# Kernel tuning notes

Measured on AMD Instinct MI355X. Metric: run time of the kernel, lower is better.

Reference implementation:

```python
import jax, jax.numpy as jnp
import numpy as np

B, S, D, H = 4, 2048, 1024, 16
HD = D // H  # head_dim = 64


def setup_inputs() -> dict:
    key = jax.random.key(0)
    ks = jax.random.split(key, 10)
    scale = 1.0 / np.sqrt(D)
    x = jax.random.normal(ks[0], (B, S, D), dtype=jnp.float32)
    mask = jax.random.randint(ks[1], (B, S, S), 0, 2, dtype=jnp.int32)
    Wq = jax.random.normal(ks[2], (D, D), dtype=jnp.float32) * scale
    Wk = jax.random.normal(ks[3], (D, D), dtype=jnp.float32) * scale
    Wv = jax.random.normal(ks[4], (D, D), dtype=jnp.float32) * scale
    Wo = jax.random.normal(ks[5], (D, D), dtype=jnp.float32) * scale
    bq = jax.random.normal(ks[6], (D,), dtype=jnp.float32) * 0.01
    bk = jax.random.normal(ks[7], (D,), dtype=jnp.float32) * 0.01
    bv = jax.random.normal(ks[8], (D,), dtype=jnp.float32) * 0.01
    bo = jax.random.normal(ks[9], (D,), dtype=jnp.float32) * 0.01
    return {"x": x, "mask": mask, "Wq": Wq, "bq": bq, "Wk": Wk, "bk": bk,
            "Wv": Wv, "bv": bv, "Wo": Wo, "bo": bo}


def reference(x, mask, Wq, bq, Wk, bk, Wv, bv, Wo, bo):
    # QKV projections (nn.Linear: x @ W^T + b; W stored pre-transposed here as [D,D])
    q = x @ Wq + bq  # [B,S,D]
    k = x @ Wk + bk
    v = x @ Wv + bv
    # split heads -> [B,H,S,HD]
    def heads(t):
        return t.reshape(B, S, H, HD).transpose(0, 2, 1, 3)
    q, k, v = heads(q), heads(k), heads(v)
    scores = jnp.einsum('bhqd,bhkd->bhqk', q, k) / jnp.sqrt(jnp.float32(HD))
    # mask: [B,S,S] -> broadcast over heads; positions where mask==0 get -inf
    scores = jnp.where(mask[:, None, :, :] == 0, -jnp.inf, scores)
    attn = jax.nn.softmax(scores, axis=-1)
    attn = jnp.where(jnp.isnan(attn), 0.0, attn)  # nan_to_num(nan=0.0)
    out = jnp.einsum('bhqk,bhkd->bhqd', attn, v)  # [B,H,S,HD]
    out = out.transpose(0, 2, 1, 3).reshape(B, S, D)
    return out @ Wo + bo
```

## Files before the change

### kernel.cpp

```cpp
#include <hip/hip_runtime.h>
#include <hip/hip_bf16.h>
#include <stdint.h>

#define B_  4
#define S_  2048
#define D_  1024
#define H_  16
#define HD_ 64

typedef __attribute__((ext_vector_type(4))) float f32x4;
typedef __attribute__((ext_vector_type(8))) short bf16x8;

typedef const unsigned int __attribute__((address_space(1)))* gas_ptr;
typedef unsigned int __attribute__((address_space(3)))* las_ptr;

__device__ __forceinline__ void async16(const void* g, void* l) {
  __builtin_amdgcn_global_load_lds((gas_ptr)g, (las_ptr)l, 16, 0, 0);
}

__global__ __launch_bounds__(256) void cvt_x(const float* __restrict__ in,
                                             __hip_bfloat16* __restrict__ out,
                                             int n) {
  const int i = (blockIdx.x * blockDim.x + threadIdx.x) * 4;
  if (i >= n) return;
  const float4 v = *(const float4*)(in + i);
  union { ushort4 u; __hip_bfloat16 h[4]; } o;
  o.h[0] = (__hip_bfloat16)v.x;
  o.h[1] = (__hip_bfloat16)v.y;
  o.h[2] = (__hip_bfloat16)v.z;
  o.h[3] = (__hip_bfloat16)v.w;
  *(ushort4*)(out + i) = o.u;
}

__global__ __launch_bounds__(256) void pack_mask(const int* __restrict__ mk,
                                                 unsigned long long* __restrict__ bits) {
  const long long i = (long long)blockIdx.x * 256 + threadIdx.x;
  const unsigned long long b = __ballot(mk[i] != 0);
  if ((threadIdx.x & 63) == 0) bits[i >> 6] = b;
}

__global__ void transpose_w(const float* __restrict__ Wq,
                            const float* __restrict__ Wk,
                            const float* __restrict__ Wv,
                            const float* __restrict__ Wo,
                            __hip_bfloat16* __restrict__ Wt_qkv,
                            __hip_bfloat16* __restrict__ Wt_o) {
  __shared__ float t[32][33];
  const int z = blockIdx.z;
  const float* W = (z == 0) ? Wq : (z == 1) ? Wk : (z == 2) ? Wv : Wo;
  __hip_bfloat16* Wt = (z < 3) ? (Wt_qkv + (size_t)z * D_ * D_) : Wt_o;
  const int x = blockIdx.x * 32 + threadIdx.x;
  const int y = blockIdx.y * 32 + threadIdx.y;
  t[threadIdx.y][threadIdx.x] = W[(size_t)y * D_ + x];
  __syncthreads();
  const int xo = blockIdx.y * 32 + threadIdx.x;
  const int yo = blockIdx.x * 32 + threadIdx.y;
  Wt[(size_t)yo * D_ + xo] = (__hip_bfloat16)t[threadIdx.x][threadIdx.y];
}

__global__ __launch_bounds__(256) void gemm_qkv(
    const __hip_bfloat16* __restrict__ A,
    const __hip_bfloat16* __restrict__ Bt,
    const float* __restrict__ bq,
    const float* __restrict__ bk,
    const float* __restrict__ bv,
    __hip_bfloat16* __restrict__ QKo,
    __hip_bfloat16* __restrict__ Vt) {
  __shared__ __hip_bfloat16 sA[128 * 32];
  __shared__ __hip_bfloat16 sB[128 * 32];
  const int K = 1024;
  const int tid  = threadIdx.x;
  const int wave = tid >> 6;
  const int lane = tid & 63;
  const int quad = lane >> 4;
  const int l16  = lane & 15;
  const int bm = blockIdx.y * 128;
  const int bn = blockIdx.x * 128;
  const int wm = (wave >> 1) * 64;
  const int wn = (wave & 1) * 64;

  const int r0 = wave * 2, r1 = wave * 2 + 1;
  const int lrow = lane >> 2;
  const int lcol = (lane & 3) * 8;

  const __hip_bfloat16* ga0 = A  + (size_t)(bm + r0 * 16 + lrow) * K + lcol;
  const __hip_bfloat16* ga1 = A  + (size_t)(bm + r1 * 16 + lrow) * K + lcol;
  const __hip_bfloat16* gb0 = Bt + (size_t)(bn + r0 * 16 + lrow) * K + lcol;
  const __hip_bfloat16* gb1 = Bt + (size_t)(bn + r1 * 16 + lrow) * K + lcol;
  char* la0 = (char*)sA + r0 * 1024;
  char* la1 = (char*)sA + r1 * 1024;
  char* lb0 = (char*)sB + r0 * 1024;
  char* lb1 = (char*)sB + r1 * 1024;

  const char* pa = (const char*)sA + (wm + l16) * 64 + quad * 16;
  const char* pb = (const char*)sB + (wn + l16) * 64 + quad * 16;

  f32x4 acc[4][4] = {};

  for (int k0 = 0; k0 < K; k0 += 32) {
    async16(ga0 + k0, la0);
    async16(ga1 + k0, la1);
    async16(gb0 + k0, lb0);
    async16(gb1 + k0, lb1);
    __syncthreads();
    bf16x8 af[4], bf[4];
#pragma unroll
    for (int mt = 0; mt < 4; ++mt) af[mt] = *(const bf16x8*)(pa + mt * 1024);
#pragma unroll
    for (int nt = 0; nt < 4; ++nt) bf[nt] = *(const bf16x8*)(pb + nt * 1024);
#pragma unroll
    for (int mt = 0; mt < 4; ++mt)
#pragma unroll
      for (int nt = 0; nt < 4; ++nt)
        acc[mt][nt] = __builtin_amdgcn_mfma_f32_16x16x32_bf16(af[mt], bf[nt], acc[mt][nt], 0, 0, 0);
    __syncthreads();
  }

#pragma unroll
  for (int mt = 0; mt < 4; ++mt) {
    const int row = bm + wm + mt * 16 + quad * 4;
#pragma unroll
    for (int nt = 0; nt < 4; ++nt) {
      const int col = bn + wn + nt * 16 + l16;
      f32x4 v = acc[mt][nt];
      if (col < 2048) {
        const float bias = (col < 1024) ? bq[col] : bk[col - 1024];
        const float sc = (col < 1024) ? 0.18033688011f : 1.0f;
#pragma unroll
        for (int r = 0; r < 4; ++r)
          QKo[(size_t)(row + r) * 2048 + col] = (__hip_bfloat16)((v[r] + bias) * sc);
      } else {
        const int cv = col - 2048;
        const float bias = bv[cv];
        const int hh = cv >> 6, d = cv & 63;
        const int bb = row >> 11, s0 = row & 2047;
        union { __hip_bfloat16 h[4]; unsigned long long u; } pk;
#pragma unroll
        for (int r = 0; r < 4; ++r) pk.h[r] = (__hip_bfloat16)(v[r] + bias);
        *(unsigned long long*)(Vt + ((size_t)(bb * 16 + hh) * 64 + d) * 2048 + s0) = pk.u;
      }
    }
  }
}

__global__ __launch_bounds__(256) void gemm_out(
    const __hip_bfloat16* __restrict__ A,
    const __hip_bfloat16* __restrict__ Bt,
    const float* __restrict__ b0,
    float* __restrict__ C,
    int N, int K) {
  __shared__ __hip_bfloat16 sA[128 * 32];
  __shared__ __hip_bfloat16 sB[128 * 32];
  const int tid  = threadIdx.x;
  const int wave = tid >> 6;
  const int lane = tid & 63;
  const int quad = lane >> 4;
  const int l16  = lane & 15;
  const int bm = blockIdx.y * 128;
  const int bn = blockIdx.x * 128;
  const int wm = (wave >> 1) * 64;
  const int wn = (wave & 1) * 64;

  const int r0 = wave * 2, r1 = wave * 2 + 1;
  const int lrow = lane >> 2;
  const int lcol = (lane & 3) * 8;

  const __hip_bfloat16* ga0 = A  + (size_t)(bm + r0 * 16 + lrow) * K + lcol;
  const __hip_bfloat16* ga1 = A  + (size_t)(bm + r1 * 16 + lrow) * K + lcol;
  const __hip_bfloat16* gb0 = Bt + (size_t)(bn + r0 * 16 + lrow) * K + lcol;
  const __hip_bfloat16* gb1 = Bt + (size_t)(bn + r1 * 16 + lrow) * K + lcol;
  char* la0 = (char*)sA + r0 * 1024;
  char* la1 = (char*)sA + r1 * 1024;
  char* lb0 = (char*)sB + r0 * 1024;
  char* lb1 = (char*)sB + r1 * 1024;

  const char* pa = (const char*)sA + (wm + l16) * 64 + quad * 16;
  const char* pb = (const char*)sB + (wn + l16) * 64 + quad * 16;

  f32x4 acc[4][4] = {};

  for (int k0 = 0; k0 < K; k0 += 32) {
    async16(ga0 + k0, la0);
    async16(ga1 + k0, la1);
    async16(gb0 + k0, lb0);
    async16(gb1 + k0, lb1);
    __syncthreads();
    bf16x8 af[4], bf[4];
#pragma unroll
    for (int mt = 0; mt < 4; ++mt) af[mt] = *(const bf16x8*)(pa + mt * 1024);
#pragma unroll
    for (int nt = 0; nt < 4; ++nt) bf[nt] = *(const bf16x8*)(pb + nt * 1024);
#pragma unroll
    for (int mt = 0; mt < 4; ++mt)
#pragma unroll
      for (int nt = 0; nt < 4; ++nt)
        acc[mt][nt] = __builtin_amdgcn_mfma_f32_16x16x32_bf16(af[mt], bf[nt], acc[mt][nt], 0, 0, 0);
    __syncthreads();
  }

#pragma unroll
  for (int mt = 0; mt < 4; ++mt) {
    const int row = bm + wm + mt * 16 + quad * 4;
#pragma unroll
    for (int nt = 0; nt < 4; ++nt) {
      const int col = bn + wn + nt * 16 + l16;
      const float bias = b0[col];
      f32x4 v = acc[mt][nt];
#pragma unroll
      for (int r = 0; r < 4; ++r)
        C[(size_t)(row + r) * N + col] = v[r] + bias;
    }
  }
}

__global__ __launch_bounds__(256, 4) void flash_attn(
    const __hip_bfloat16* __restrict__ QK,
    const __hip_bfloat16* __restrict__ Vt,
    const unsigned long long* __restrict__ mbits,
    __hip_bfloat16* __restrict__ O) {
  __shared__ __hip_bfloat16 sK[2][64 * 64];
  __shared__ __hip_bfloat16 sV[2][64 * 64];

  const int qt = blockIdx.x, h = blockIdx.y, b = blockIdx.z;
  const int tid = threadIdx.x;
  const int wave = tid >> 6, lane = tid & 63, quad = lane >> 4, l16 = lane & 15;
  const int qbase = qt * 128;
  const size_t brow = (size_t)b * S_;
  const int bh = b * H_ + h;

  bf16x8 qf[2][2];
#pragma unroll
  for (int g = 0; g < 2; ++g) {
    const __hip_bfloat16* qrow =
        QK + (brow + qbase + g * 64 + wave * 16 + l16) * 2048 + h * 64;
#pragma unroll
    for (int c = 0; c < 2; ++c)
      qf[g][c] = *(const bf16x8*)(qrow + c * 32 + quad * 8);
  }

  const int srow = lane >> 3;
  const int schk = (lane & 7) ^ srow;
  const __hip_bfloat16* gk0 =
      QK + (brow + wave * 16 + srow) * 2048 + 1024 + h * 64 + schk * 8;
  const __hip_bfloat16* gk1 = gk0 + (size_t)8 * 2048;
  const __hip_bfloat16* gv0 =
      Vt + ((size_t)bh * 64 + wave * 16 + srow) * 2048 + schk * 8;
  const __hip_bfloat16* gv1 = gv0 + (size_t)8 * 2048;
  char* const lK[2] = {(char*)&sK[0][0] + wave * 2048, (char*)&sK[1][0] + wave * 2048};
  char* const lV[2] = {(char*)&sV[0][0] + wave * 2048, (char*)&sV[1][0] + wave * 2048};

  const unsigned long long* mb0 = mbits + (brow + qbase + wave * 16 + l16) * 32;
  const unsigned long long* mb1 = mb0 + (size_t)64 * 32;

  const int xl = l16 & 7;
  const int koff0 = ((quad ^ xl) * 16);
  const int rowb = l16 * 128;

  float lst[2] = {0.f, 0.f};
  f32x4 oacc[2][4] = {};

  async16(gk0, lK[0]);
  async16(gk1, lK[0] + 1024);
  async16(gv0, lV[0]);
  async16(gv1, lV[0] + 1024);
  unsigned long long pm0 = mb0[0], pm1 = mb1[0];
  gk0 += (size_t)64 * 2048; gk1 += (size_t)64 * 2048;
  gv0 += 64; gv1 += 64;
  __syncthreads();

  const int NT = S_ / 64;
  for (int kt = 0; kt < NT; ++kt) {
    const int cur = kt & 1, nxt = cur ^ 1;

    if (kt + 1 < NT) {
      async16(gk0, lK[nxt]);
      async16(gk1, lK[nxt] + 1024);
      async16(gv0, lV[nxt]);
      async16(gv1, lV[nxt] + 1024);
      gk0 += (size_t)64 * 2048; gk1 += (size_t)64 * 2048;
      gv0 += 64; gv1 += 64;
    }
    const unsigned long long mw0 = pm0;
    const unsigned long long mw1 = pm1;
    const int kn = (kt + 1 < NT) ? kt + 1 : kt;
    pm0 = mb0[kn];
    pm1 = mb1[kn];

    const char* bK = (const char*)&sK[cur][0] + rowb;
    unsigned pl[2][4][2];
    float ps[2][4];
#pragma unroll
    for (int mt = 0; mt < 4; ++mt) {
      const bf16x8 kf0 = *(const bf16x8*)(bK + mt * 2048 + koff0);
      const bf16x8 kf1 = *(const bf16x8*)(bK + mt * 2048 + (koff0 ^ 64));
      f32x4 a0 = {}, a1 = {};
      __builtin_amdgcn_s_setprio(1);
      a0 = __builtin_amdgcn_mfma_f32_16x16x32_bf16(kf0, qf[0][0], a0, 0, 0, 0);
      a0 = __builtin_amdgcn_mfma_f32_16x16x32_bf16(kf1, qf[0][1], a0, 0, 0, 0);
      a1 = __builtin_amdgcn_mfma_f32_16x16x32_bf16(kf0, qf[1][0], a1, 0, 0, 0);
      a1 = __builtin_amdgcn_mfma_f32_16x16x32_bf16(kf1, qf[1][1], a1, 0, 0, 0);
      __builtin_amdgcn_s_setprio(0);
#pragma unroll
      for (int g = 0; g < 2; ++g) {
        const unsigned long long mw = g ? mw1 : mw0;
        const unsigned w32 =
            ((mt < 2) ? (unsigned)mw : (unsigned)(mw >> 32)) >> (quad * 4);
        const f32x4 av = g ? a1 : a0;
        float pr[4];
#pragma unroll
        for (int r = 0; r < 4; ++r) {
          const float p = __builtin_amdgcn_exp2f(av[r]);
          pr[r] = ((w32 >> ((mt & 1) * 16 + r)) & 1u) ? p : 0.f;
        }
        union { __hip_bfloat16 h[2]; unsigned u; } c0, c1;
        c0.h[0] = (__hip_bfloat16)pr[0]; c0.h[1] = (__hip_bfloat16)pr[1];
        c1.h[0] = (__hip_bfloat16)pr[2]; c1.h[1] = (__hip_bfloat16)pr[3];
        pl[g][mt][0] = c0.u;
        pl[g][mt][1] = c1.u;
        ps[g][mt] = (pr[0] + pr[1]) + (pr[2] + pr[3]);
      }
    }
    lst[0] += (ps[0][0] + ps[0][1]) + (ps[0][2] + ps[0][3]);
    lst[1] += (ps[1][0] + ps[1][1]) + (ps[1][2] + ps[1][3]);

    bf16x8 pf[2][2];
#pragma unroll
    for (int g = 0; g < 2; ++g)
#pragma unroll
      for (int c = 0; c < 2; ++c) {
        unsigned e0 = pl[g][2 * c][0], o0 = pl[g][2 * c + 1][0];
        unsigned e1 = pl[g][2 * c][1], o1 = pl[g][2 * c + 1][1];
        asm("v_permlane32_swap_b32 %0, %1" : "+v"(e0), "+v"(o0));
        asm("v_permlane16_swap_b32 %0, %1" : "+v"(e0), "+v"(o0));
        asm("v_permlane32_swap_b32 %0, %1" : "+v"(e1), "+v"(o1));
        asm("v_permlane16_swap_b32 %0, %1" : "+v"(e1), "+v"(o1));
        union { unsigned u[4]; bf16x8 v; } uu;
        uu.u[0] = e0; uu.u[1] = e1; uu.u[2] = o0; uu.u[3] = o1;
        pf[g][c] = uu.v;
      }

    const char* bV = (const char*)&sV[cur][0] + rowb;
    __builtin_amdgcn_s_setprio(1);
#pragma unroll
    for (int ht = 0; ht < 4; ++ht) {
      const bf16x8 vf0 = *(const bf16x8*)(bV + ht * 2048 + koff0);
      const bf16x8 vf1 = *(const bf16x8*)(bV + ht * 2048 + (koff0 ^ 64));
      oacc[0][ht] = __builtin_amdgcn_mfma_f32_16x16x32_bf16(vf0, pf[0][0], oacc[0][ht], 0, 0, 0);
      oacc[0][ht] = __builtin_amdgcn_mfma_f32_16x16x32_bf16(vf1, pf[0][1], oacc[0][ht], 0, 0, 0);
      oacc[1][ht] = __builtin_amdgcn_mfma_f32_16x16x32_bf16(vf0, pf[1][0], oacc[1][ht], 0, 0, 0);
      oacc[1][ht] = __builtin_amdgcn_mfma_f32_16x16x32_bf16(vf1, pf[1][1], oacc[1][ht], 0, 0, 0);
    }
    __builtin_amdgcn_s_setprio(0);

    __syncthreads();
  }

#pragma unroll
  for (int g = 0; g < 2; ++g) {
    float l = lst[g];
    l += __shfl_xor(l, 16);
    l += __shfl_xor(l, 32);
    const float inv = (l > 0.f) ? 1.f / l : 0.f;
    __hip_bfloat16* orow =
        O + (brow + qbase + g * 64 + wave * 16 + l16) * 1024 + h * 64;
#pragma unroll
    for (int ht = 0; ht < 4; ++ht) {
      union { __hip_bfloat16 h[4]; unsigned long long u; } ok_;
#pragma unroll
      for (int r = 0; r < 4; ++r) ok_.h[r] = (__hip_bfloat16)(oacc[g][ht][r] * inv);
      *(unsigned long long*)(orow + ht * 16 + quad * 4) = ok_.u;
    }
  }
}

extern "C" void kernel_launch(void* const* d_in, const int* in_sizes, int n_in,
                              void* d_out, int out_size, void* d_ws, size_t ws_size,
                              hipStream_t stream) {
  const float* x  = (const float*)d_in[0];
  const int*   mk = (const int*)d_in[1];
  const float* Wq = (const float*)d_in[2];
  const float* bq = (const float*)d_in[3];
  const float* Wk = (const float*)d_in[4];
  const float* bk = (const float*)d_in[5];
  const float* Wv = (const float*)d_in[6];
  const float* bv = (const float*)d_in[7];
  const float* Wo = (const float*)d_in[8];
  const float* bo = (const float*)d_in[9];
  float* out = (float*)d_out;

  __hip_bfloat16* X16    = (__hip_bfloat16*)d_ws;
  __hip_bfloat16* Wt_qkv = X16 + (size_t)B_ * S_ * D_;
  __hip_bfloat16* Wt_o   = Wt_qkv + (size_t)3 * D_ * D_;
  __hip_bfloat16* QK     = Wt_o + (size_t)D_ * D_;
  __hip_bfloat16* Vt     = QK + (size_t)B_ * S_ * 2 * D_;
  __hip_bfloat16* Obuf   = Vt + (size_t)B_ * H_ * HD_ * S_;
  unsigned long long* mbits = (unsigned long long*)(Obuf + (size_t)B_ * S_ * D_);

  const int nx = B_ * S_ * D_;
  cvt_x<<<dim3((nx / 4 + 255) / 256), 256, 0, stream>>>(x, X16, nx);
  transpose_w<<<dim3(32, 32, 4), dim3(32, 32), 0, stream>>>(Wq, Wk, Wv, Wo, Wt_qkv, Wt_o);
  pack_mask<<<dim3((int)((size_t)B_ * S_ * S_ / 256)), 256, 0, stream>>>(mk, mbits);
  gemm_qkv<<<dim3(3 * D_ / 128, B_ * S_ / 128), 256, 0, stream>>>(
      X16, Wt_qkv, bq, bk, bv, QK, Vt);
  flash_attn<<<dim3(S_ / 128, H_, B_), 256, 0, stream>>>(QK, Vt, mbits, Obuf);
  gemm_out<<<dim3(D_ / 128, B_ * S_ / 128), 256, 0, stream>>>(
      Obuf, Wt_o, bo, out, D_, D_);
}
```

Baseline: 390.4 us.

## Pre-expand mask into bf16 AND-masks and compute row sums with MFMA

Replaces the 1-bit packed mask with a pre-expanded 16-bit-per-element mask, laid out to match the MFMA fragment order. The attention kernel can then apply the mask with a bitwise AND on packed bf16 probabilities instead of per-element bit tests and selects. The softmax row-sum is moved from scalar adds plus cross-lane shuffles to extra MFMAs against a ones vector. The cost is 16x more mask bytes to write and read (about 64 MB instead of 4 MB), plus four extra MFMAs per tile. The sum is now taken from the bf16-rounded probabilities, which slightly changes numerics.

Measured after the change: 363.5 us. -6.9%, faster.

```diff
diff --git a/kernel.cpp b/kernel.cpp
--- a/kernel.cpp
+++ b/kernel.cpp
@@ -32,11 +32,18 @@
   *(ushort4*)(out + i) = o.u;
 }
 
-__global__ __launch_bounds__(256) void pack_mask(const int* __restrict__ mk,
-                                                 unsigned long long* __restrict__ bits) {
-  const long long i = (long long)blockIdx.x * 256 + threadIdx.x;
-  const unsigned long long b = __ballot(mk[i] != 0);
-  if ((threadIdx.x & 63) == 0) bits[i >> 6] = b;
+__global__ __launch_bounds__(256) void expand_mask(const int* __restrict__ mk,
+                                                   uint2* __restrict__ xm) {
+  const unsigned j = blockIdx.x * 256 + threadIdx.x;
+  const int mt = j & 3, quad = (j >> 2) & 3, kt = (j >> 4) & 31;
+  const int q = (j >> 9) & 2047, b = j >> 20;
+  const size_t row = (size_t)b * 2048 + q;
+  const int key = kt * 64 + mt * 16 + quad * 4;
+  const int4 m = *(const int4*)(mk + row * 2048 + key);
+  uint2 o;
+  o.x = (m.x ? 0xFFFFu : 0u) | (m.y ? 0xFFFF0000u : 0u);
+  o.y = (m.z ? 0xFFFFu : 0u) | (m.w ? 0xFFFF0000u : 0u);
+  xm[j] = o;
 }
 
 __global__ void transpose_w(const float* __restrict__ Wq,
@@ -216,7 +223,7 @@
 __global__ __launch_bounds__(256, 4) void flash_attn(
     const __hip_bfloat16* __restrict__ QK,
     const __hip_bfloat16* __restrict__ Vt,
-    const unsigned long long* __restrict__ mbits,
+    const uint4* __restrict__ XM,
     __hip_bfloat16* __restrict__ O) {
   __shared__ __hip_bfloat16 sK[2][64 * 64];
   __shared__ __hip_bfloat16 sV[2][64 * 64];
@@ -249,21 +256,23 @@
   char* const lK[2] = {(char*)&sK[0][0] + wave * 2048, (char*)&sK[1][0] + wave * 2048};
   char* const lV[2] = {(char*)&sV[0][0] + wave * 2048, (char*)&sV[1][0] + wave * 2048};
 
-  const unsigned long long* mb0 = mbits + (brow + qbase + wave * 16 + l16) * 32;
-  const unsigned long long* mb1 = mb0 + (size_t)64 * 32;
+  const uint4* xpa = XM + ((brow + qbase + wave * 16 + l16) * 256 + quad * 2);
+  const uint4* xpb = xpa + (size_t)64 * 256;
 
   const int xl = l16 & 7;
   const int koff0 = ((quad ^ xl) * 16);
   const int rowb = l16 * 128;
 
-  float lst[2] = {0.f, 0.f};
+  const bf16x8 onesv = {(short)0x3F80, (short)0x3F80, (short)0x3F80, (short)0x3F80,
+                        (short)0x3F80, (short)0x3F80, (short)0x3F80, (short)0x3F80};
+  f32x4 lacc[2] = {};
   f32x4 oacc[2][4] = {};
 
   async16(gk0, lK[0]);
   async16(gk1, lK[0] + 1024);
   async16(gv0, lV[0]);
   async16(gv1, lV[0] + 1024);
-  unsigned long long pm0 = mb0[0], pm1 = mb1[0];
+  uint4 x0a = xpa[0], x1a = xpa[1], x0b = xpb[0], x1b = xpb[1];
   gk0 += (size_t)64 * 2048; gk1 += (size_t)64 * 2048;
   gv0 += 64; gv1 += 64;
   __syncthreads();
@@ -280,15 +289,13 @@
       gk0 += (size_t)64 * 2048; gk1 += (size_t)64 * 2048;
       gv0 += 64; gv1 += 64;
     }
-    const unsigned long long mw0 = pm0;
-    const unsigned long long mw1 = pm1;
+    const uint4 ca0 = x0a, ca1 = x1a, cb0 = x0b, cb1 = x1b;
     const int kn = (kt + 1 < NT) ? kt + 1 : kt;
-    pm0 = mb0[kn];
-    pm1 = mb1[kn];
+    x0a = xpa[kn * 8]; x1a = xpa[kn * 8 + 1];
+    x0b = xpb[kn * 8]; x1b = xpb[kn * 8 + 1];
 
     const char* bK = (const char*)&sK[cur][0] + rowb;
     unsigned pl[2][4][2];
-    float ps[2][4];
 #pragma unroll
     for (int mt = 0; mt < 4; ++mt) {
       const bf16x8 kf0 = *(const bf16x8*)(bK + mt * 2048 + koff0);
@@ -302,26 +309,19 @@
       __builtin_amdgcn_s_setprio(0);
 #pragma unroll
       for (int g = 0; g < 2; ++g) {
-        const unsigned long long mw = g ? mw1 : mw0;
-        const unsigned w32 =
-            ((mt < 2) ? (unsigned)mw : (unsigned)(mw >> 32)) >> (quad * 4);
+        const uint4 cc = g ? ((mt < 2) ? cb0 : cb1) : ((mt < 2) ? ca0 : ca1);
+        const unsigned w0 = (mt & 1) ? cc.z : cc.x;
+        const unsigned w1 = (mt & 1) ? cc.w : cc.y;
         const f32x4 av = g ? a1 : a0;
-        float pr[4];
-#pragma unroll
-        for (int r = 0; r < 4; ++r) {
-          const float p = __builtin_amdgcn_exp2f(av[r]);
-          pr[r] = ((w32 >> ((mt & 1) * 16 + r)) & 1u) ? p : 0.f;
-        }
         union { __hip_bfloat16 h[2]; unsigned u; } c0, c1;
-        c0.h[0] = (__hip_bfloat16)pr[0]; c0.h[1] = (__hip_bfloat16)pr[1];
-        c1.h[0] = (__hip_bfloat16)pr[2]; c1.h[1] = (__hip_bfloat16)pr[3];
-        pl[g][mt][0] = c0.u;
-        pl[g][mt][1] = c1.u;
-        ps[g][mt] = (pr[0] + pr[1]) + (pr[2] + pr[3]);
+        c0.h[0] = (__hip_bfloat16)__builtin_amdgcn_exp2f(av[0]);
+        c0.h[1] = (__hip_bfloat16)__builtin_amdgcn_exp2f(av[1]);
+        c1.h[0] = (__hip_bfloat16)__builtin_amdgcn_exp2f(av[2]);
+        c1.h[1] = (__hip_bfloat16)__builtin_amdgcn_exp2f(av[3]);
+        pl[g][mt][0] = c0.u & w0;
+        pl[g][mt][1] = c1.u & w1;
       }
     }
-    lst[0] += (ps[0][0] + ps[0][1]) + (ps[0][2] + ps[0][3]);
-    lst[1] += (ps[1][0] + ps[1][1]) + (ps[1][2] + ps[1][3]);
 
     bf16x8 pf[2][2];
 #pragma unroll
@@ -350,6 +350,10 @@
       oacc[1][ht] = __builtin_amdgcn_mfma_f32_16x16x32_bf16(vf0, pf[1][0], oacc[1][ht], 0, 0, 0);
       oacc[1][ht] = __builtin_amdgcn_mfma_f32_16x16x32_bf16(vf1, pf[1][1], oacc[1][ht], 0, 0, 0);
     }
+    lacc[0] = __builtin_amdgcn_mfma_f32_16x16x32_bf16(onesv, pf[0][0], lacc[0], 0, 0, 0);
+    lacc[0] = __builtin_amdgcn_mfma_f32_16x16x32_bf16(onesv, pf[0][1], lacc[0], 0, 0, 0);
+    lacc[1] = __builtin_amdgcn_mfma_f32_16x16x32_bf16(onesv, pf[1][0], lacc[1], 0, 0, 0);
+    lacc[1] = __builtin_amdgcn_mfma_f32_16x16x32_bf16(onesv, pf[1][1], lacc[1], 0, 0, 0);
     __builtin_amdgcn_s_setprio(0);
 
     __syncthreads();
@@ -357,9 +361,7 @@
 
 #pragma unroll
   for (int g = 0; g < 2; ++g) {
-    float l = lst[g];
-    l += __shfl_xor(l, 16);
-    l += __shfl_xor(l, 32);
+    const float l = lacc[g][0];
     const float inv = (l > 0.f) ? 1.f / l : 0.f;
     __hip_bfloat16* orow =
         O + (brow + qbase + g * 64 + wave * 16 + l16) * 1024 + h * 64;
@@ -394,15 +396,17 @@
   __hip_bfloat16* QK     = Wt_o + (size_t)D_ * D_;
   __hip_bfloat16* Vt     = QK + (size_t)B_ * S_ * 2 * D_;
   __hip_bfloat16* Obuf   = Vt + (size_t)B_ * H_ * HD_ * S_;
-  unsigned long long* mbits = (unsigned long long*)(Obuf + (size_t)B_ * S_ * D_);
+  unsigned* xmask = (unsigned*)(Obuf + (size_t)B_ * S_ * D_);
 
   const int nx = B_ * S_ * D_;
   cvt_x<<<dim3((nx / 4 + 255) / 256), 256, 0, stream>>>(x, X16, nx);
   transpose_w<<<dim3(32, 32, 4), dim3(32, 32), 0, stream>>>(Wq, Wk, Wv, Wo, Wt_qkv, Wt_o);
-  pack_mask<<<dim3((int)((size_t)B_ * S_ * S_ / 256)), 256, 0, stream>>>(mk, mbits);
+  expand_mask<<<dim3((int)((size_t)B_ * S_ * S_ / 4 / 256)), 256, 0, stream>>>(
+      mk, (uint2*)xmask);
   gemm_qkv<<<dim3(3 * D_ / 128, B_ * S_ / 128), 256, 0, stream>>>(
       X16, Wt_qkv, bq, bk, bv, QK, Vt);
-  flash_attn<<<dim3(S_ / 128, H_, B_), 256, 0, stream>>>(QK, Vt, mbits, Obuf);
+  flash_attn<<<dim3(S_ / 128, H_, B_), 256, 0, stream>>>(
+      QK, Vt, (const uint4*)xmask, Obuf);
   gemm_out<<<dim3(D_ / 128, B_ * S_ / 128), 256, 0, stream>>>(
       Obuf, Wt_o, bo, out, D_, D_);
 }
```
